# Optimization experiments

Hardware: AMD Instinct MI355X
Metric: run time of the kernel (lower is better)

The kernel has to match this reference:

```python
import jax, jax.numpy as jnp
import numpy as np

NEG_INF = jnp.finfo(jnp.float32).min


def setup_inputs() -> dict:
    key = jax.random.key(0)
    ks = jax.random.split(key, 8)
    B, C, V = 64, 2048, 256
    ART = 2048
    D = C + ART        # 4096, classifier input
    F = 4096           # feature_size
    OUT = 1000         # out_channels
    x = jax.random.normal(ks[0], (B, C, V), dtype=jnp.float32)
    x_art = jax.random.normal(ks[1], (B, ART, V), dtype=jnp.float32)
    list_length = jax.random.randint(ks[2], (B,), 1, V + 1, dtype=jnp.int32)
    w1 = jax.random.normal(ks[3], (D, F), dtype=jnp.float32) * 0.02
    b1 = jnp.zeros((F,), dtype=jnp.float32)
    w2 = jax.random.normal(ks[4], (F, F), dtype=jnp.float32) * 0.02
    b2 = jnp.zeros((F,), dtype=jnp.float32)
    w3 = jax.random.normal(ks[5], (F, OUT), dtype=jnp.float32) * 0.02
    b3 = jnp.zeros((OUT,), dtype=jnp.float32)
    return {"x": x, "x_art": x_art, "list_length": list_length,
            "w1": w1, "b1": b1, "w2": w2, "b2": b2, "w3": w3, "b3": b3}


def reference(x, x_art, list_length, w1, b1, w2, b2, w3, b3):
    # x: [B, C, V], x_art: [B, ART, V] -> feats [B, V, C+ART]
    feats = jnp.concatenate((jnp.swapaxes(x, 1, 2), jnp.swapaxes(x_art, 1, 2)), axis=-1)
    B, V, D = feats.shape
    # Ragged max over views: view 0 is always included in the torch loop,
    # so effective length = max(list_length, 1).
    lens = jnp.maximum(list_length, 1)
    mask = jnp.arange(V, dtype=jnp.int32)[None, :] < lens[:, None]  # [B, V]
    pooled = jnp.max(jnp.where(mask[:, :, None], feats, NEG_INF), axis=1)  # [B, D]
    # Classifier MLP (dropout is identity at inference)
    h = jax.nn.relu(pooled @ w1 + b1)
    h = jax.nn.relu(h @ w2 + b2)
    return h @ w3 + b3
```

## Files before the change

kernel.cpp:

```cpp
#include <hip/hip_runtime.h>
#include <cfloat>

#define BB 64
#define CC 2048
#define AR 2048
#define DD 4096
#define VV 256
#define FF 4096
#define OO 1000

__global__ __launch_bounds__(256) void pool_kernel(
    const float* __restrict__ x, const float* __restrict__ xart,
    const int* __restrict__ ll, float* __restrict__ pooledT)
{
    int waveId = (blockIdx.x * 256 + threadIdx.x) >> 6;
    int lane   = threadIdx.x & 63;
    int row0   = waveId * 32;
    int b  = row0 >> 12;
    int d0 = row0 & 4095;
    int len = ll[b];
    if (len < 1) len = 1;
    const float* base = (d0 < CC)
        ? (x    + ((size_t)b * CC + d0)        * VV)
        : (xart + ((size_t)b * AR + (d0 - CC)) * VV);
    int v0  = lane * 4;
    int rem = len - v0;

    for (int r = 0; r < 32; r += 4) {
        const float* s = base + (size_t)r * VV;
        float m0 = -FLT_MAX, m1 = -FLT_MAX, m2 = -FLT_MAX, m3 = -FLT_MAX;
        if (rem > 0) {
            float4 a0 = *(const float4*)(s + v0);
            float4 a1 = *(const float4*)(s + VV + v0);
            float4 a2 = *(const float4*)(s + 2 * VV + v0);
            float4 a3 = *(const float4*)(s + 3 * VV + v0);
            m0 = a0.x; m1 = a1.x; m2 = a2.x; m3 = a3.x;
            if (rem > 1) { m0 = fmaxf(m0, a0.y); m1 = fmaxf(m1, a1.y);
                           m2 = fmaxf(m2, a2.y); m3 = fmaxf(m3, a3.y); }
            if (rem > 2) { m0 = fmaxf(m0, a0.z); m1 = fmaxf(m1, a1.z);
                           m2 = fmaxf(m2, a2.z); m3 = fmaxf(m3, a3.z); }
            if (rem > 3) { m0 = fmaxf(m0, a0.w); m1 = fmaxf(m1, a1.w);
                           m2 = fmaxf(m2, a2.w); m3 = fmaxf(m3, a3.w); }
        }
        #pragma unroll
        for (int off = 32; off > 0; off >>= 1) {
            m0 = fmaxf(m0, __shfl_xor(m0, off, 64));
            m1 = fmaxf(m1, __shfl_xor(m1, off, 64));
            m2 = fmaxf(m2, __shfl_xor(m2, off, 64));
            m3 = fmaxf(m3, __shfl_xor(m3, off, 64));
        }
        float wv = m0;
        if (lane == 1) wv = m1;
        else if (lane == 2) wv = m2;
        else if (lane == 3) wv = m3;
        if (lane < 4)
            pooledT[(size_t)(d0 + r + lane) * 64 + b] = wv;
    }
}

__global__ __launch_bounds__(256) void gemm_partial(
    const float* __restrict__ P, const float* __restrict__ W,
    float* __restrict__ part, int F, int kchunk)
{
    __shared__ float lds_p[16][64];
    __shared__ float lds_w[16][128];
    int t  = threadIdx.x;
    int tx = t & 15, ty = t >> 4;
    int f0 = blockIdx.x * 128;
    int k0 = blockIdx.y * kchunk;
    int stages = kchunk >> 4;
    int c1 = f0 + tx * 4;
    int c2 = f0 + 64 + tx * 4;
    bool v2 = (c2 + 3 < F) || (c2 + 4 == F);

    float acc[4][8];
    #pragma unroll
    for (int i = 0; i < 4; ++i)
        #pragma unroll
        for (int j = 0; j < 8; ++j) acc[i][j] = 0.f;

    int k = k0 + ty;
    float4 pv  = *(const float4*)(P + (size_t)k * 64 + tx * 4);
    const float* wr = W + (size_t)k * F;
    float4 wv0 = *(const float4*)(wr + c1);
    float4 wv1;
    if (v2) wv1 = *(const float4*)(wr + c2);
    else {
        wv1.x = (c2     < F) ? wr[c2]     : 0.f;
        wv1.y = (c2 + 1 < F) ? wr[c2 + 1] : 0.f;
        wv1.z = (c2 + 2 < F) ? wr[c2 + 2] : 0.f;
        wv1.w = (c2 + 3 < F) ? wr[c2 + 3] : 0.f;
    }

    for (int s = 0; s < stages; ++s) {
        __syncthreads();
        *(float4*)&lds_p[ty][tx * 4]      = pv;
        *(float4*)&lds_w[ty][tx * 4]      = wv0;
        *(float4*)&lds_w[ty][64 + tx * 4] = wv1;
        __syncthreads();
        if (s + 1 < stages) {
            int kn = k0 + (s + 1) * 16 + ty;
            pv = *(const float4*)(P + (size_t)kn * 64 + tx * 4);
            const float* wrn = W + (size_t)kn * F;
            wv0 = *(const float4*)(wrn + c1);
            if (v2) wv1 = *(const float4*)(wrn + c2);
            else {
                wv1.x = (c2     < F) ? wrn[c2]     : 0.f;
                wv1.y = (c2 + 1 < F) ? wrn[c2 + 1] : 0.f;
                wv1.z = (c2 + 2 < F) ? wrn[c2 + 2] : 0.f;
                wv1.w = (c2 + 3 < F) ? wrn[c2 + 3] : 0.f;
            }
        }
        #pragma unroll
        for (int kk = 0; kk < 16; ++kk) {
            float4 p4 = *(const float4*)&lds_p[kk][ty * 4];
            float4 wa = *(const float4*)&lds_w[kk][tx * 4];
            float4 wb = *(const float4*)&lds_w[kk][64 + tx * 4];
            #pragma unroll
            for (int i = 0; i < 4; ++i) {
                float pi = (i == 0) ? p4.x : (i == 1) ? p4.y : (i == 2) ? p4.z : p4.w;
                acc[i][0] += pi * wa.x;  acc[i][1] += pi * wa.y;
                acc[i][2] += pi * wa.z;  acc[i][3] += pi * wa.w;
                acc[i][4] += pi * wb.x;  acc[i][5] += pi * wb.y;
                acc[i][6] += pi * wb.z;  acc[i][7] += pi * wb.w;
            }
        }
    }

    float* dst = part + (size_t)(blockIdx.y * 64) * F;
    #pragma unroll
    for (int i = 0; i < 4; ++i) {
        float* r = dst + (size_t)(ty * 4 + i) * F;
        *(float4*)(r + c1) = make_float4(acc[i][0], acc[i][1], acc[i][2], acc[i][3]);
        if (v2)
            *(float4*)(r + c2) = make_float4(acc[i][4], acc[i][5], acc[i][6], acc[i][7]);
        else {
            if (c2     < F) r[c2]     = acc[i][4];
            if (c2 + 1 < F) r[c2 + 1] = acc[i][5];
            if (c2 + 2 < F) r[c2 + 2] = acc[i][6];
            if (c2 + 3 < F) r[c2 + 3] = acc[i][7];
        }
    }
}

__global__ __launch_bounds__(256) void reduce_bias_relu_T(
    const float* __restrict__ part, const float* __restrict__ bias,
    float* __restrict__ outT, int nchunk, int F)
{
    __shared__ float lds[64 * 17];
    int t  = threadIdx.x;
    int f0 = blockIdx.x * 16;
    int fl = t & 15;
    int ty = t >> 4;
    float bv = bias[f0 + fl];
    float acc[4];
    #pragma unroll
    for (int j = 0; j < 4; ++j) acc[j] = bv;
    for (int c = 0; c < nchunk; ++c) {
        const float* p = part + ((size_t)c * 64) * F + f0 + fl;
        #pragma unroll
        for (int j = 0; j < 4; ++j) {
            int b = j * 16 + ty;
            acc[j] += p[(size_t)b * F];
        }
    }
    #pragma unroll
    for (int j = 0; j < 4; ++j) {
        int b = j * 16 + ty;
        lds[b * 17 + fl] = fmaxf(acc[j], 0.f);
    }
    __syncthreads();
    #pragma unroll
    for (int j = 0; j < 4; ++j) {
        int idx = j * 256 + t;
        int f = idx >> 6;
        int b = idx & 63;
        outT[(size_t)(f0 + f) * 64 + b] = lds[b * 17 + f];
    }
}

__global__ __launch_bounds__(256) void reduce_out_kernel(
    const float* __restrict__ part, const float* __restrict__ bias,
    float* __restrict__ out, int nchunk)
{
    int idx = blockIdx.x * 256 + threadIdx.x;
    if (idx >= BB * OO) return;
    int b = idx / OO, f = idx - b * OO;
    float v = bias[f];
    const float* p = part + (size_t)b * OO + f;
    #pragma unroll 8
    for (int c = 0; c < nchunk; ++c)
        v += p[(size_t)c * 64 * OO];
    out[idx] = v;
}

extern "C" void kernel_launch(void* const* d_in, const int* in_sizes, int n_in,
                              void* d_out, int out_size, void* d_ws, size_t ws_size,
                              hipStream_t stream) {
    const float* x    = (const float*)d_in[0];
    const float* xart = (const float*)d_in[1];
    const int*   ll   = (const int*)d_in[2];
    const float* w1   = (const float*)d_in[3];
    const float* b1   = (const float*)d_in[4];
    const float* w2   = (const float*)d_in[5];
    const float* b2   = (const float*)d_in[6];
    const float* w3   = (const float*)d_in[7];
    const float* b3   = (const float*)d_in[8];
    float* out = (float*)d_out;

    float* pooledT = (float*)d_ws;
    float* h1T     = pooledT + (size_t)DD * 64;
    float* h2T     = h1T     + (size_t)FF * 64;
    float* part    = h2T     + (size_t)FF * 64;

    size_t actBytes = (size_t)(DD + FF + FF) * 64 * sizeof(float);
    size_t avail    = (ws_size > actBytes) ? ws_size - actBytes : 0;
    size_t plane1   = (size_t)64 * FF * sizeof(float);
    int nk1 = 8;
    if (avail >= 32 * plane1)      nk1 = 32;
    else if (avail >= 16 * plane1) nk1 = 16;
    size_t plane3 = (size_t)64 * OO * sizeof(float);
    int nk3 = (avail >= 64 * plane3) ? 64 : 32;
    int kchunk1 = DD / nk1;
    int kchunk3 = FF / nk3;

    pool_kernel<<<2048, 256, 0, stream>>>(x, xart, ll, pooledT);

    gemm_partial<<<dim3(32, nk1), 256, 0, stream>>>(pooledT, w1, part, FF, kchunk1);
    reduce_bias_relu_T<<<FF / 16, 256, 0, stream>>>(part, b1, h1T, nk1, FF);

    gemm_partial<<<dim3(32, nk1), 256, 0, stream>>>(h1T, w2, part, FF, kchunk1);
    reduce_bias_relu_T<<<FF / 16, 256, 0, stream>>>(part, b2, h2T, nk1, FF);

    gemm_partial<<<dim3(8, nk3), 256, 0, stream>>>(h2T, w3, part, OO, kchunk3);
    reduce_out_kernel<<<(BB * OO + 255) / 256, 256, 0, stream>>>(part, b3, out, nk3);
}
```

Baseline: 420.9 us.

## Add double-buffered wide-tile GEMM for hidden layers and widen pooling rows

Adds a gemm_wide kernel for the two 4096x4096-scale layers. Each block covers 256 output columns and each thread computes an 8x8 register tile instead of 4x8. Shared memory is double-buffered, so the next stage's global loads overlap compute and only one barrier runs per stage. This raises arithmetic intensity per LDS read and halves the block count. The pooling kernel now handles 8 rows per iteration, giving more loads in flight, at the cost of more registers.

```diff
diff --git a/kernel.cpp b/kernel.cpp
--- a/kernel.cpp
+++ b/kernel.cpp
@@ -26,35 +26,125 @@
     int v0  = lane * 4;
     int rem = len - v0;
 
-    for (int r = 0; r < 32; r += 4) {
+    for (int r = 0; r < 32; r += 8) {
         const float* s = base + (size_t)r * VV;
-        float m0 = -FLT_MAX, m1 = -FLT_MAX, m2 = -FLT_MAX, m3 = -FLT_MAX;
+        float m[8];
+        #pragma unroll
+        for (int j = 0; j < 8; ++j) m[j] = -FLT_MAX;
         if (rem > 0) {
-            float4 a0 = *(const float4*)(s + v0);
-            float4 a1 = *(const float4*)(s + VV + v0);
-            float4 a2 = *(const float4*)(s + 2 * VV + v0);
-            float4 a3 = *(const float4*)(s + 3 * VV + v0);
-            m0 = a0.x; m1 = a1.x; m2 = a2.x; m3 = a3.x;
-            if (rem > 1) { m0 = fmaxf(m0, a0.y); m1 = fmaxf(m1, a1.y);
-                           m2 = fmaxf(m2, a2.y); m3 = fmaxf(m3, a3.y); }
-            if (rem > 2) { m0 = fmaxf(m0, a0.z); m1 = fmaxf(m1, a1.z);
-                           m2 = fmaxf(m2, a2.z); m3 = fmaxf(m3, a3.z); }
-            if (rem > 3) { m0 = fmaxf(m0, a0.w); m1 = fmaxf(m1, a1.w);
-                           m2 = fmaxf(m2, a2.w); m3 = fmaxf(m3, a3.w); }
+            float4 a[8];
+            #pragma unroll
+            for (int j = 0; j < 8; ++j) a[j] = *(const float4*)(s + j * VV + v0);
+            #pragma unroll
+            for (int j = 0; j < 8; ++j) {
+                m[j] = a[j].x;
+                if (rem > 1) m[j] = fmaxf(m[j], a[j].y);
+                if (rem > 2) m[j] = fmaxf(m[j], a[j].z);
+                if (rem > 3) m[j] = fmaxf(m[j], a[j].w);
+            }
         }
         #pragma unroll
         for (int off = 32; off > 0; off >>= 1) {
-            m0 = fmaxf(m0, __shfl_xor(m0, off, 64));
-            m1 = fmaxf(m1, __shfl_xor(m1, off, 64));
-            m2 = fmaxf(m2, __shfl_xor(m2, off, 64));
-            m3 = fmaxf(m3, __shfl_xor(m3, off, 64));
-        }
-        float wv = m0;
-        if (lane == 1) wv = m1;
-        else if (lane == 2) wv = m2;
-        else if (lane == 3) wv = m3;
-        if (lane < 4)
+            #pragma unroll
+            for (int j = 0; j < 8; ++j)
+                m[j] = fmaxf(m[j], __shfl_xor(m[j], off, 64));
+        }
+        float wv = m[0];
+        if (lane == 1) wv = m[1];
+        else if (lane == 2) wv = m[2];
+        else if (lane == 3) wv = m[3];
+        else if (lane == 4) wv = m[4];
+        else if (lane == 5) wv = m[5];
+        else if (lane == 6) wv = m[6];
+        else if (lane == 7) wv = m[7];
+        if (lane < 8)
             pooledT[(size_t)(d0 + r + lane) * 64 + b] = wv;
+    }
+}
+
+__global__ __launch_bounds__(256) void gemm_wide(
+    const float* __restrict__ P, const float* __restrict__ W,
+    float* __restrict__ part, int F, int kchunk)
+{
+    __shared__ float lds_p[2][16][64];
+    __shared__ float lds_w[2][16][256];
+    int t  = threadIdx.x;
+    int tx = t & 31;
+    int ty = t >> 5;
+    int f0 = blockIdx.x * 256;
+    int k0 = blockIdx.y * kchunk;
+    int stages = kchunk >> 4;
+
+    int sr = t >> 4;
+    int sc = (t & 15) * 4;
+
+    const float* Pg = P + (size_t)(k0 + sr) * 64 + sc;
+    const float* Wg = W + (size_t)(k0 + sr) * F + f0 + sc;
+
+    float acc[8][8];
+    #pragma unroll
+    for (int i = 0; i < 8; ++i)
+        #pragma unroll
+        for (int j = 0; j < 8; ++j) acc[i][j] = 0.f;
+
+    {
+        float4 pv  = *(const float4*)Pg;
+        float4 wv0 = *(const float4*)(Wg);
+        float4 wv1 = *(const float4*)(Wg + 64);
+        float4 wv2 = *(const float4*)(Wg + 128);
+        float4 wv3 = *(const float4*)(Wg + 192);
+        *(float4*)&lds_p[0][sr][sc]       = pv;
+        *(float4*)&lds_w[0][sr][sc]       = wv0;
+        *(float4*)&lds_w[0][sr][64 + sc]  = wv1;
+        *(float4*)&lds_w[0][sr][128 + sc] = wv2;
+        *(float4*)&lds_w[0][sr][192 + sc] = wv3;
+    }
+    __syncthreads();
+
+    for (int s = 0; s < stages; ++s) {
+        int buf = s & 1;
+        float4 pv, wv0, wv1, wv2, wv3;
+        bool more = (s + 1 < stages);
+        if (more) {
+            const float* Pn = Pg + (size_t)(s + 1) * 16 * 64;
+            const float* Wn = Wg + (size_t)(s + 1) * 16 * F;
+            pv  = *(const float4*)Pn;
+            wv0 = *(const float4*)(Wn);
+            wv1 = *(const float4*)(Wn + 64);
+            wv2 = *(const float4*)(Wn + 128);
+            wv3 = *(const float4*)(Wn + 192);
+        }
+        #pragma unroll
+        for (int kk = 0; kk < 16; ++kk) {
+            float4 p0 = *(const float4*)&lds_p[buf][kk][ty * 8];
+            float4 p1 = *(const float4*)&lds_p[buf][kk][ty * 8 + 4];
+            float4 w0 = *(const float4*)&lds_w[buf][kk][tx * 4];
+            float4 w1 = *(const float4*)&lds_w[buf][kk][128 + tx * 4];
+            float pb[8] = {p0.x, p0.y, p0.z, p0.w, p1.x, p1.y, p1.z, p1.w};
+            float wf[8] = {w0.x, w0.y, w0.z, w0.w, w1.x, w1.y, w1.z, w1.w};
+            #pragma unroll
+            for (int i = 0; i < 8; ++i)
+                #pragma unroll
+                for (int j = 0; j < 8; ++j)
+                    acc[i][j] += pb[i] * wf[j];
+        }
+        if (more) {
+            int nb = buf ^ 1;
+            *(float4*)&lds_p[nb][sr][sc]       = pv;
+            *(float4*)&lds_w[nb][sr][sc]       = wv0;
+            *(float4*)&lds_w[nb][sr][64 + sc]  = wv1;
+            *(float4*)&lds_w[nb][sr][128 + sc] = wv2;
+            *(float4*)&lds_w[nb][sr][192 + sc] = wv3;
+            __syncthreads();
+        }
+    }
+
+    float* dst = part + (size_t)blockIdx.y * 64 * F;
+    #pragma unroll
+    for (int i = 0; i < 8; ++i) {
+        float* r = dst + (size_t)(ty * 8 + i) * F + f0;
+        *(float4*)(r + tx * 4)       = make_float4(acc[i][0], acc[i][1], acc[i][2], acc[i][3]);
+        *(float4*)(r + 128 + tx * 4) = make_float4(acc[i][4], acc[i][5], acc[i][6], acc[i][7]);
     }
 }
 
@@ -71,7 +161,7 @@
     int stages = kchunk >> 4;
     int c1 = f0 + tx * 4;
     int c2 = f0 + 64 + tx * 4;
-    bool v2 = (c2 + 3 < F) || (c2 + 4 == F);
+    bool v2 = (c2 + 3 < F);
 
     float acc[4][8];
     #pragma unroll
@@ -127,7 +217,7 @@
         }
     }
 
-    float* dst = part + (size_t)(blockIdx.y * 64) * F;
+    float* dst = part + (size_t)blockIdx.y * 64 * F;
     #pragma unroll
     for (int i = 0; i < 4; ++i) {
         float* r = dst + (size_t)(ty * 4 + i) * F;
@@ -159,16 +249,12 @@
     for (int c = 0; c < nchunk; ++c) {
         const float* p = part + ((size_t)c * 64) * F + f0 + fl;
         #pragma unroll
-        for (int j = 0; j < 4; ++j) {
-            int b = j * 16 + ty;
-            acc[j] += p[(size_t)b * F];
-        }
-    }
-    #pragma unroll
-    for (int j = 0; j < 4; ++j) {
-        int b = j * 16 + ty;
-        lds[b * 17 + fl] = fmaxf(acc[j], 0.f);
-    }
+        for (int j = 0; j < 4; ++j)
+            acc[j] += p[(size_t)(j * 16 + ty) * F];
+    }
+    #pragma unroll
+    for (int j = 0; j < 4; ++j)
+        lds[(j * 16 + ty) * 17 + fl] = fmaxf(acc[j], 0.f);
     __syncthreads();
     #pragma unroll
     for (int j = 0; j < 4; ++j) {
@@ -226,10 +312,10 @@
 
     pool_kernel<<<2048, 256, 0, stream>>>(x, xart, ll, pooledT);
 
-    gemm_partial<<<dim3(32, nk1), 256, 0, stream>>>(pooledT, w1, part, FF, kchunk1);
+    gemm_wide<<<dim3(FF / 256, nk1), 256, 0, stream>>>(pooledT, w1, part, FF, kchunk1);
     reduce_bias_relu_T<<<FF / 16, 256, 0, stream>>>(part, b1, h1T, nk1, FF);
 
-    gemm_partial<<<dim3(32, nk1), 256, 0, stream>>>(h1T, w2, part, FF, kchunk1);
+    gemm_wide<<<dim3(FF / 256, nk1), 256, 0, stream>>>(h1T, w2, part, FF, kchunk1);
     reduce_bias_relu_T<<<FF / 16, 256, 0, stream>>>(part, b2, h2T, nk1, FF);
 
     gemm_partial<<<dim3(8, nk3), 256, 0, stream>>>(h2T, w3, part, OO, kchunk3);
```

New measurement: 439.0 us. 4.3% more time.
